# Optimization experiments

Hardware: AMD Instinct MI355X
Metric: run time of the kernel (lower is better)

Reference implementation:

```python
import jax, jax.numpy as jnp
import numpy as np

NB = 5  # frequency bands


def _ln(x, g, b, eps=1e-5):
    m = jnp.mean(x, axis=-1, keepdims=True)
    v = jnp.var(x, axis=-1, keepdims=True)
    return (x - m) / jnp.sqrt(v + eps) * g + b


def _graph_adj(x, adj_w, sw1, sb1, sw2, sb2, pos_factor, pos_enc):
    # x: [B, D, N] -> degree-normalized adjacency [B, N, N]
    d = x.shape[1]
    xt = jnp.swapaxes(x, 1, 2)  # [B, N, D]
    # concat-MLP first layer split: cat(xi, xj) @ W1 == xi @ W1[:d] + xj @ W1[d:]
    a = xt @ sw1[:d]
    bpart = xt @ sw1[d:]
    h = jax.nn.elu(a[:, :, None, :] + bpart[:, None, :, :] + sb1)  # [B, N, N, H]
    dyn = jax.nn.sigmoid(jnp.squeeze(h @ sw2, -1) + sb2)  # [B, N, N]
    static = jax.nn.softmax(adj_w, axis=-1)
    pos = jax.nn.softmax(pos_enc, axis=-1)
    comb = jax.nn.softmax(static + dyn + pos_factor * pos, axis=-1)
    deg = jnp.sum(comb, axis=-1)
    dis = (deg + 1e-8) ** -0.5
    return dis[:, :, None] * comb * dis[:, None, :]


def _gcn(x, adj, w, b):
    # x: [B, D, N], adj: [B, N, N] -> [B, D_out, N]
    xt = jnp.swapaxes(x, 1, 2)
    out = jnp.einsum('bij,bjd->bid', adj, xt) @ w + b
    return jnp.swapaxes(out, 1, 2)


def _mha(x, qkv_w, qkv_b, ow, ob, nh=4):
    B, S, D = x.shape
    dh = D // nh
    q, k, v = jnp.split(x @ qkv_w + qkv_b, 3, axis=-1)
    q = q.reshape(B, S, nh, dh)
    k = k.reshape(B, S, nh, dh)
    v = v.reshape(B, S, nh, dh)
    att = jax.nn.softmax(jnp.einsum('bihd,bjhd->bhij', q, k) / float(np.sqrt(dh)), axis=-1)
    o = jnp.einsum('bhij,bjhd->bihd', att, v).reshape(B, S, D)
    return o @ ow + ob


def setup_inputs():
    key = jax.random.key(0)
    B, D, N = 16, 256, 64
    ks = iter(jax.random.split(key, 40))

    def rn(shape, s=0.05):
        return jax.random.normal(next(ks), shape, dtype=jnp.float32) * s

    eyeN = jnp.eye(N, dtype=jnp.float32)
    return dict(
        feature=jax.random.normal(next(ks), (B, NB * D, 1, N), dtype=jnp.float32),
        l_adj_w=jnp.tile(eyeN[None], (NB, 1, 1)),
        l_sim_w1=rn((NB, 2 * D, D)), l_sim_b1=jnp.zeros((NB, D), jnp.float32),
        l_sim_w2=rn((NB, D, 1)), l_sim_b2=jnp.zeros((NB, 1), jnp.float32),
        l_pos_factor=jnp.full((NB,), 0.5, jnp.float32),
        l_pos_enc=jnp.tile(eyeN[None], (NB, 1, 1)),
        l_gcn_w=rn((NB, D, D)), l_gcn_b=jnp.zeros((NB, D), jnp.float32),
        g_adj_w=jnp.eye(NB, dtype=jnp.float32),
        g_sim_w1=rn((2 * D, D)), g_sim_b1=jnp.zeros((D,), jnp.float32),
        g_sim_w2=rn((D, 1)), g_sim_b2=jnp.zeros((1,), jnp.float32),
        g_pos_factor=jnp.float32(0.5),
        g_pos_enc=jnp.eye(NB, dtype=jnp.float32),
        g_gcn_w=rn((D, D)), g_gcn_b=jnp.zeros((D,), jnp.float32),
        qkv_w=rn((D, 3 * D)), qkv_b=jnp.zeros((3 * D,), jnp.float32),
        attn_ow=rn((D, D)), attn_ob=jnp.zeros((D,), jnp.float32),
        ln1_g=jnp.ones((D,), jnp.float32), ln1_b=jnp.zeros((D,), jnp.float32),
        ln2_g=jnp.ones((D,), jnp.float32), ln2_b=jnp.zeros((D,), jnp.float32),
        mlp_w1=rn((D, 4 * D)), mlp_b1=jnp.zeros((4 * D,), jnp.float32),
        mlp_w2=rn((4 * D, D)), mlp_b2=jnp.zeros((D,), jnp.float32),
        imp_w=rn((NB, N, 1)), imp_b=jnp.zeros((NB, 1), jnp.float32),
    )


def reference(feature, l_adj_w, l_sim_w1, l_sim_b1, l_sim_w2, l_sim_b2,
              l_pos_factor, l_pos_enc, l_gcn_w, l_gcn_b,
              g_adj_w, g_sim_w1, g_sim_b1, g_sim_w2, g_sim_b2,
              g_pos_factor, g_pos_enc, g_gcn_w, g_gcn_b,
              qkv_w, qkv_b, attn_ow, attn_ob,
              ln1_g, ln1_b, ln2_g, ln2_b,
              mlp_w1, mlp_b1, mlp_w2, mlp_b2,
              imp_w, imp_b):
    B = feature.shape[0]
    D = l_gcn_w.shape[-1]
    N = feature.shape[-1]
    # [B, 5*D, 1, N] -> [5, B, D, N] band-major
    x5 = jnp.moveaxis(feature.reshape(B, NB, D, N), 1, 0)
    # per-band local graphs + GCNs (vmapped over the 5 bands)
    local_adj = jax.vmap(_graph_adj)(x5, l_adj_w, l_sim_w1, l_sim_b1,
                                     l_sim_w2, l_sim_b2, l_pos_factor, l_pos_enc)
    local_out = jax.vmap(_gcn)(x5, local_adj, l_gcn_w, l_gcn_b)  # [5, B, D, N]
    scale_nodes = jnp.moveaxis(jnp.mean(local_out, axis=-1), 0, 1)  # [B, 5, D]
    # cross-band attention block (pre: MHA + residual + LN, then MLP + residual + LN)
    attn = _mha(scale_nodes, qkv_w, qkv_b, attn_ow, attn_ob)
    h1 = _ln(scale_nodes + attn, ln1_g, ln1_b)
    mlp = jax.nn.gelu(h1 @ mlp_w1 + mlp_b1, approximate=False) @ mlp_w2 + mlp_b2
    se = _ln(h1 + mlp, ln2_g, ln2_b)  # [B, 5, D]
    # global scale graph over the 5 band nodes
    xg = jnp.swapaxes(se, 1, 2)  # [B, D, 5]
    g_adj = _graph_adj(xg, g_adj_w, g_sim_w1, g_sim_b1, g_sim_w2, g_sim_b2,
                       g_pos_factor, g_pos_enc)
    g_out = jnp.swapaxes(_gcn(xg, g_adj, g_gcn_w, g_gcn_b), 1, 2)  # [B, 5, D]
    # modulate each local band feature by its global scale vector
    enh = local_out * jnp.moveaxis(g_out, 1, 0)[..., None]  # [5, B, D, N]
    # per-band importance projection over channels: [5, B, D, 1]
    out5 = jnp.einsum('kbdn,kno->kbdo', enh, imp_w) + imp_b[:, None, None, :]
    output = jnp.moveaxis(out5, 0, 1).reshape(B, NB * D, 1, 1)
    return output, g_adj, jnp.moveaxis(local_out, 0, 1)
```

## Files before the change

### kernel.cpp

```cpp
#include <hip/hip_runtime.h>
#include <hip/hip_bf16.h>

#define NBANDS 5
#define BATCH  16
#define DIM    256
#define NNODE  64
#define SEQ    5
#define NHEAD  4
#define DHEAD  64

typedef __hip_bfloat16 bf16;
typedef unsigned short ushort_t;
typedef __attribute__((ext_vector_type(8))) short short8;
typedef __attribute__((ext_vector_type(4))) float float4v;

__device__ __forceinline__ float bu2f(ushort_t u){
    bf16 h = *reinterpret_cast<bf16*>(&u);
    return __bfloat162float(h);
}
__device__ __forceinline__ ushort_t f2bu(float x){
    bf16 h = __float2bfloat16(x);
    return *reinterpret_cast<ushort_t*>(&h);
}

__global__ void __launch_bounds__(256) k_head(
    const float* __restrict__ l_adj_w, const float* __restrict__ l_pos_enc,
    const float* __restrict__ l_pf,
    const float* __restrict__ g_adj_w, const float* __restrict__ g_pos_enc,
    const float* __restrict__ g_pf,
    float* __restrict__ sbase, float* __restrict__ gbase,
    const float* __restrict__ w1, const float* __restrict__ gw,
    ushort_t* __restrict__ w1bt, ushort_t* __restrict__ gwbt,
    const float* __restrict__ feat,
    ushort_t* __restrict__ xtb, ushort_t* __restrict__ xtT)
{
    int blk = blockIdx.x;
    int tid = threadIdx.x;
    __shared__ ushort_t tile[64][65];

    if (blk < 80) {
        int r = blk*4 + (tid>>6);
        int k = r >> 6, i = r & 63;
        int t = tid & 63;
        float aw = l_adj_w[(k*NNODE + i)*NNODE + t];
        float pe = l_pos_enc[(k*NNODE + i)*NNODE + t];
        float m1 = aw, m2 = pe;
        for (int o=32;o>0;o>>=1){ m1 = fmaxf(m1, __shfl_xor(m1,o,64)); m2 = fmaxf(m2, __shfl_xor(m2,o,64)); }
        float e1 = __expf(aw-m1), e2 = __expf(pe-m2);
        float s1=e1, s2=e2;
        for (int o=32;o>0;o>>=1){ s1 += __shfl_xor(s1,o,64); s2 += __shfl_xor(s2,o,64); }
        float pf = l_pf[k];
        sbase[(k*NNODE+i)*NNODE + t] = e1/s1 + pf*(e2/s2);
    } else if (blk == 80) {
        if (tid < NBANDS) {
            int i = tid;
            float r1[NBANDS], r2[NBANDS];
            float m1=-1e30f, m2=-1e30f;
            for (int j=0;j<NBANDS;j++){
                r1[j]=g_adj_w[i*NBANDS+j]; r2[j]=g_pos_enc[i*NBANDS+j];
                m1=fmaxf(m1,r1[j]); m2=fmaxf(m2,r2[j]);
            }
            float s1=0.f,s2=0.f;
            for (int j=0;j<NBANDS;j++){ r1[j]=__expf(r1[j]-m1); r2[j]=__expf(r2[j]-m2); s1+=r1[j]; s2+=r2[j]; }
            float pf = g_pf[0];
            for (int j=0;j<NBANDS;j++) gbase[i*NBANDS+j] = r1[j]/s1 + pf*(r2[j]/s2);
        }
    } else if (blk < 321) {
        int idx = blk - 81;
        int inst = idx >> 4;
        int t = idx & 15;
        int r0 = (t>>2)*64, c0 = (t&3)*64;
        const float* src; ushort_t* dst;
        if (inst < 10){
            int k = inst>>1, half = inst&1;
            src = w1  + ((size_t)k*512 + half*256)*256;
            dst = w1bt+ ((size_t)k*512 + half*256)*256;
        } else {
            int k = inst-10;
            src = gw  + (size_t)k*65536;
            dst = gwbt+ (size_t)k*65536;
        }
        int jj = tid & 63, i4 = tid >> 6;
        for (int p=0;p<16;p++){
            int i = p*4 + i4;
            tile[i][jj] = f2bu(src[(size_t)(r0+i)*256 + c0 + jj]);
        }
        __syncthreads();
        for (int p=0;p<16;p++){
            int i = p*4 + i4;
            dst[(size_t)(c0+i)*256 + r0 + jj] = tile[jj][i];
        }
    } else {
        int idx = blk - 321;
        int k = idx / BATCH, b = idx % BATCH;
        const float* src = feat + ((size_t)b*NBANDS*DIM + (size_t)k*DIM)*NNODE;
        ushort_t* dst = xtb + (size_t)(k*BATCH+b)*NNODE*DIM;
        ushort_t* dstT = xtT + (size_t)(k*BATCH+b)*DIM*NNODE;
        for (int u=0; u<64; ++u){
            int i = u*256 + tid;
            dstT[i] = f2bu(src[i]);
        }
        for (int dt=0; dt<4; ++dt){
            for (int r=0;r<16;r++){
                int dp = r*4 + (tid>>6);
                int n  = tid & 63;
                tile[dp][n] = f2bu(src[(size_t)(dt*64+dp)*NNODE + n]);
            }
            __syncthreads();
            for (int r=0;r<16;r++){
                int n  = r*4 + (tid>>6);
                int dp = tid & 63;
                dst[(size_t)n*DIM + dt*64 + dp] = tile[dp][n];
            }
            __syncthreads();
        }
    }
}

__global__ void __launch_bounds__(256) k_ab_mfma(const ushort_t* __restrict__ xtb,
                        const ushort_t* __restrict__ w1bt, const float* __restrict__ b1,
                        ushort_t* __restrict__ aab, ushort_t* __restrict__ bbb)
{
    int blk = blockIdx.x;
    int kband = blk / (BATCH*8);
    int b = (blk/8) % BATCH;
    int nblk = blk & 7;
    int tid = threadIdx.x;
    int wave = tid>>6, lane = tid&63;
    int c16 = lane & 15, quad = lane >> 4;
    int m0 = wave*16;
    size_t rowbase = (size_t)(kband*BATCH+b)*NNODE;
    const ushort_t* Aptr = xtb + (rowbase + m0 + c16)*DIM + quad*8;
    const ushort_t* Bbase = w1bt + (size_t)kband*512*DIM;
    int ncol0 = nblk*64;
    const ushort_t* Bptr0 = Bbase + (size_t)(ncol0 +  0 + c16)*DIM + quad*8;
    const ushort_t* Bptr1 = Bbase + (size_t)(ncol0 + 16 + c16)*DIM + quad*8;
    const ushort_t* Bptr2 = Bbase + (size_t)(ncol0 + 32 + c16)*DIM + quad*8;
    const ushort_t* Bptr3 = Bbase + (size_t)(ncol0 + 48 + c16)*DIM + quad*8;
    float4v acc0 = {0.f,0.f,0.f,0.f}, acc1 = acc0, acc2 = acc0, acc3 = acc0;
    #pragma unroll
    for (int ks=0; ks<8; ++ks){
        short8 a  = *reinterpret_cast<const short8*>(Aptr  + ks*32);
        short8 b0 = *reinterpret_cast<const short8*>(Bptr0 + ks*32);
        short8 b1v= *reinterpret_cast<const short8*>(Bptr1 + ks*32);
        short8 b2 = *reinterpret_cast<const short8*>(Bptr2 + ks*32);
        short8 b3 = *reinterpret_cast<const short8*>(Bptr3 + ks*32);
        acc0 = __builtin_amdgcn_mfma_f32_16x16x32_bf16(a, b0, acc0, 0,0,0);
        acc1 = __builtin_amdgcn_mfma_f32_16x16x32_bf16(a, b1v, acc1, 0,0,0);
        acc2 = __builtin_amdgcn_mfma_f32_16x16x32_bf16(a, b2, acc2, 0,0,0);
        acc3 = __builtin_amdgcn_mfma_f32_16x16x32_bf16(a, b3, acc3, 0,0,0);
    }
    int half = nblk >> 2;
    int cbase = (nblk & 3)*64;
    ushort_t* dst = half ? bbb : aab;
    float4v accs[4] = {acc0, acc1, acc2, acc3};
    #pragma unroll
    for (int nt=0; nt<4; ++nt){
        int cg = cbase + nt*16 + c16;
        float bias = half ? 0.f : b1[kband*DIM + cg];
        #pragma unroll
        for (int r=0;r<4;r++){
            int m = m0 + quad*4 + r;
            dst[(rowbase + m)*DIM + cg] = f2bu(accs[nt][r] + bias);
        }
    }
}

__global__ void __launch_bounds__(256) k_dyn_comb(const ushort_t* __restrict__ aab,
                           const ushort_t* __restrict__ bbb,
                           const float* __restrict__ w2, const float* __restrict__ b2arr,
                           const float* __restrict__ sbase,
                           ushort_t* __restrict__ combb)
{
    int blk = blockIdx.x;
    int k = blk / (BATCH*16);
    int b = (blk / 16) % BATCH;
    int i0 = (blk % 16) * 4;
    int kb = k*BATCH + b;
    __shared__ ushort_t bs[64][260];
    __shared__ float arows[4][DIM];
    __shared__ float w2s[DIM];
    int tid = threadIdx.x;
    int wave = tid >> 6, lane = tid & 63;
    const ushort_t* bsrc = bbb + (size_t)kb*NNODE*DIM;
    for (int u=0; u<16; ++u){
        int idx = u*1024 + tid*4;
        int row = idx >> 8, col = idx & 255;
        *reinterpret_cast<ushort4*>(&bs[row][col]) =
            *reinterpret_cast<const ushort4*>(&bsrc[(size_t)row*DIM + col]);
    }
    for (int r=0;r<4;r++) arows[r][tid] = bu2f(aab[((size_t)kb*NNODE + i0 + r)*DIM + tid]);
    w2s[tid] = w2[k*DIM + tid];
    __syncthreads();

    int i = i0 + wave;
    float acc = 0.f;
    #pragma unroll 4
    for (int dd=0; dd<64; ++dd){
        ushort4 bv = *reinterpret_cast<const ushort4*>(&bs[lane][dd*4]);
        float4 av = *reinterpret_cast<const float4*>(&arows[wave][dd*4]);
        float4 wv = *reinterpret_cast<const float4*>(&w2s[dd*4]);
        float v0 = av.x + bu2f(bv.x);
        float v1 = av.y + bu2f(bv.y);
        float v2 = av.z + bu2f(bv.z);
        float v3 = av.w + bu2f(bv.w);
        float e0 = (v0>0.f)? v0 : (__expf(v0)-1.f);
        float e1 = (v1>0.f)? v1 : (__expf(v1)-1.f);
        float e2 = (v2>0.f)? v2 : (__expf(v2)-1.f);
        float e3 = (v3>0.f)? v3 : (__expf(v3)-1.f);
        acc += e0*wv.x + e1*wv.y + e2*wv.z + e3*wv.w;
    }
    float sb2 = b2arr[k];
    float sg = 1.f/(1.f + __expf(-(acc + sb2)));
    float val = sbase[(k*NNODE + i)*NNODE + lane] + sg;
    float m = val;
    for (int o=32;o>0;o>>=1) m = fmaxf(m, __shfl_xor(m,o,64));
    float e = __expf(val - m);
    float s = e;
    for (int o=32;o>0;o>>=1) s += __shfl_xor(s,o,64);
    combb[((size_t)kb*NNODE + i)*NNODE + lane] = f2bu(e/s);
}

__global__ void __launch_bounds__(256) k_y_mfma(const ushort_t* __restrict__ combb,
                       const ushort_t* __restrict__ xtT,
                       ushort_t* __restrict__ yb)
{
    int blk = blockIdx.x;
    int kband = blk / (BATCH*4);
    int b = (blk/4) % BATCH;
    int nblk = blk & 3;
    int tid = threadIdx.x;
    int wave = tid>>6, lane = tid&63;
    int c16 = lane & 15, quad = lane >> 4;
    int m0 = wave*16;
    int kb = kband*BATCH + b;
    const ushort_t* Aptr = combb + ((size_t)kb*NNODE + m0 + c16)*NNODE + quad*8;
    const ushort_t* Bbase = xtT + (size_t)kb*DIM*NNODE;
    int ncol0 = nblk*64;
    const ushort_t* Bptr0 = Bbase + (size_t)(ncol0 +  0 + c16)*NNODE + quad*8;
    const ushort_t* Bptr1 = Bbase + (size_t)(ncol0 + 16 + c16)*NNODE + quad*8;
    const ushort_t* Bptr2 = Bbase + (size_t)(ncol0 + 32 + c16)*NNODE + quad*8;
    const ushort_t* Bptr3 = Bbase + (size_t)(ncol0 + 48 + c16)*NNODE + quad*8;
    float4v acc0 = {0.f,0.f,0.f,0.f}, acc1 = acc0, acc2 = acc0, acc3 = acc0;
    #pragma unroll
    for (int ks=0; ks<2; ++ks){
        short8 a  = *reinterpret_cast<const short8*>(Aptr  + ks*32);
        short8 b0 = *reinterpret_cast<const short8*>(Bptr0 + ks*32);
        short8 b1v= *reinterpret_cast<const short8*>(Bptr1 + ks*32);
        short8 b2 = *reinterpret_cast<const short8*>(Bptr2 + ks*32);
        short8 b3 = *reinterpret_cast<const short8*>(Bptr3 + ks*32);
        acc0 = __builtin_amdgcn_mfma_f32_16x16x32_bf16(a, b0, acc0, 0,0,0);
        acc1 = __builtin_amdgcn_mfma_f32_16x16x32_bf16(a, b1v, acc1, 0,0,0);
        acc2 = __builtin_amdgcn_mfma_f32_16x16x32_bf16(a, b2, acc2, 0,0,0);
        acc3 = __builtin_amdgcn_mfma_f32_16x16x32_bf16(a, b3, acc3, 0,0,0);
    }
    size_t rowbase = (size_t)kb*NNODE;
    float4v accs[4] = {acc0, acc1, acc2, acc3};
    #pragma unroll
    for (int nt=0; nt<4; ++nt){
        int cg = ncol0 + nt*16 + c16;
        #pragma unroll
        for (int r=0;r<4;r++){
            int m = m0 + quad*4 + r;
            yb[(rowbase + m)*DIM + cg] = f2bu(accs[nt][r]);
        }
    }
}

__global__ void __launch_bounds__(256) k_gcn_mfma(const ushort_t* __restrict__ yb,
                         const ushort_t* __restrict__ gwbt, const float* __restrict__ gb,
                         float* __restrict__ out_local)
{
    int blk = blockIdx.x;
    int kband = blk / (BATCH*4);
    int b = (blk/4) % BATCH;
    int nblk = blk & 3;
    int tid = threadIdx.x;
    int wave = tid>>6, lane = tid&63;
    int c16 = lane & 15, quad = lane >> 4;
    int m0 = wave*16;
    int kb = kband*BATCH + b;
    const ushort_t* Aptr = yb + ((size_t)kb*NNODE + m0 + c16)*DIM + quad*8;
    const ushort_t* Bbase = gwbt + (size_t)kband*DIM*DIM;
    int ncol0 = nblk*64;
    const ushort_t* Bptr0 = Bbase + (size_t)(ncol0 +  0 + c16)*DIM + quad*8;
    const ushort_t* Bptr1 = Bbase + (size_t)(ncol0 + 16 + c16)*DIM + quad*8;
    const ushort_t* Bptr2 = Bbase + (size_t)(ncol0 + 32 + c16)*DIM + quad*8;
    const ushort_t* Bptr3 = Bbase + (size_t)(ncol0 + 48 + c16)*DIM + quad*8;
    float4v acc0 = {0.f,0.f,0.f,0.f}, acc1 = acc0, acc2 = acc0, acc3 = acc0;
    #pragma unroll
    for (int ks=0; ks<8; ++ks){
        short8 a  = *reinterpret_cast<const short8*>(Aptr  + ks*32);
        short8 b0 = *reinterpret_cast<const short8*>(Bptr0 + ks*32);
        short8 b1v= *reinterpret_cast<const short8*>(Bptr1 + ks*32);
        short8 b2 = *reinterpret_cast<const short8*>(Bptr2 + ks*32);
        short8 b3 = *reinterpret_cast<const short8*>(Bptr3 + ks*32);
        acc0 = __builtin_amdgcn_mfma_f32_16x16x32_bf16(a, b0, acc0, 0,0,0);
        acc1 = __builtin_amdgcn_mfma_f32_16x16x32_bf16(a, b1v, acc1, 0,0,0);
        acc2 = __builtin_amdgcn_mfma_f32_16x16x32_bf16(a, b2, acc2, 0,0,0);
        acc3 = __builtin_amdgcn_mfma_f32_16x16x32_bf16(a, b3, acc3, 0,0,0);
    }
    float4v accs[4] = {acc0, acc1, acc2, acc3};
    #pragma unroll
    for (int nt=0; nt<4; ++nt){
        int cg = ncol0 + nt*16 + c16;
        float bias = gb[kband*DIM + cg];
        float4 v = make_float4(accs[nt][0]+bias, accs[nt][1]+bias, accs[nt][2]+bias, accs[nt][3]+bias);
        float* dst = out_local + ((size_t)(b*NBANDS + kband)*DIM + cg)*NNODE + m0 + quad*4;
        *reinterpret_cast<float4*>(dst) = v;
    }
}

__global__ void k_scale2(const float* __restrict__ out_local, const float* __restrict__ imp_w,
                         float* __restrict__ scalew, float* __restrict__ impw)
{
    int k = blockIdx.x / BATCH, b = blockIdx.x % BATCH;
    int d = threadIdx.x;
    __shared__ float iw[NNODE];
    if (d < NNODE) iw[d] = imp_w[k*NNODE + d];
    __syncthreads();
    const float4* zl = reinterpret_cast<const float4*>(out_local + ((size_t)(b*NBANDS + k)*DIM + d)*NNODE);
    float s = 0.f, di = 0.f;
    #pragma unroll
    for (int q=0;q<16;++q){
        float4 v = zl[q];
        s  += v.x + v.y + v.z + v.w;
        di += v.x*iw[q*4] + v.y*iw[q*4+1] + v.z*iw[q*4+2] + v.w*iw[q*4+3];
    }
    scalew[((size_t)b*SEQ + k)*DIM + d] = s * (1.f/64.f);
    impw[((size_t)b*SEQ + k)*DIM + d]   = di;
}

template<int COLS, int SLICES>
__global__ void __launch_bounds__(256) k_gemv(const float* __restrict__ x, const float* __restrict__ w,
                       const float* __restrict__ bias, float* __restrict__ out,
                       int K, int N, int act)
{
    int chunks = N / COLS;
    int row = blockIdx.x / chunks;
    int n0 = (blockIdx.x % chunks) * COLS;
    int c = threadIdx.x % COLS, s = threadIdx.x / COLS;
    __shared__ float xs[1024];
    __shared__ float part[SLICES][COLS];
    for (int i = threadIdx.x; i < K; i += 256) xs[i] = x[(size_t)row*K + i];
    __syncthreads();
    int klen = K / SLICES;
    const float* wp = w + (size_t)(s*klen)*N + n0 + c;
    const float* xp = xs + s*klen;
    float acc = 0.f;
    #pragma unroll 8
    for (int i = 0; i < klen; ++i) acc += xp[i] * wp[(size_t)i*N];
    part[s][c] = acc;
    __syncthreads();
    if (s == 0){
        float v = bias[n0+c];
        #pragma unroll
        for (int q=0;q<SLICES;q++) v += part[q][c];
        if (act) v = 0.5f*v*(1.f + erff(v*0.70710678118654752f));
        out[(size_t)row*N + n0 + c] = v;
    }
}

__global__ void k_attn(const float* __restrict__ qkvw, float* __restrict__ ows)
{
    int b = blockIdx.x;
    int tid = threadIdx.x;
    int h = tid >> 6, l = tid & 63;
    __shared__ float att[NHEAD][SEQ][SEQ];
    const float* base = qkvw + (size_t)b*SEQ*3*DIM;
    for (int i=0;i<SEQ;i++){
        float qv = base[(size_t)i*3*DIM + h*DHEAD + l];
        for (int j=0;j<SEQ;j++){
            float kv = base[(size_t)j*3*DIM + DIM + h*DHEAD + l];
            float p = qv * kv;
            for (int o=32;o>0;o>>=1) p += __shfl_xor(p,o,64);
            if (l==0) att[h][i][j] = p * 0.125f;
        }
    }
    __syncthreads();
    if (l == 0){
        for (int i=0;i<SEQ;i++){
            float m=-1e30f;
            for (int j=0;j<SEQ;j++) m = fmaxf(m, att[h][i][j]);
            float e[SEQ]; float s=0.f;
            for (int j=0;j<SEQ;j++){ e[j] = __expf(att[h][i][j]-m); s+=e[j]; }
            for (int j=0;j<SEQ;j++) att[h][i][j] = e[j]/s;
        }
    }
    __syncthreads();
    for (int i=0;i<SEQ;i++){
        float acc=0.f;
        for (int j=0;j<SEQ;j++) acc += att[h][i][j] * base[(size_t)j*3*DIM + 2*DIM + h*DHEAD + l];
        ows[((size_t)b*SEQ + i)*DIM + h*DHEAD + l] = acc;
    }
}

__device__ __forceinline__ float block_ln(float v, int tid, float* red, float g, float bln)
{
    float s = v;
    for (int o=32;o>0;o>>=1) s += __shfl_xor(s,o,64);
    int wave = tid>>6, lane = tid&63;
    if (lane==0) red[wave] = s;
    __syncthreads();
    float mean = (red[0]+red[1]+red[2]+red[3]) * (1.f/DIM);
    float c = v - mean;
    float q = c*c;
    for (int o=32;o>0;o>>=1) q += __shfl_xor(q,o,64);
    __syncthreads();
    if (lane==0) red[wave] = q;
    __syncthreads();
    float var = (red[0]+red[1]+red[2]+red[3]) * (1.f/DIM);
    return c * rsqrtf(var + 1e-5f) * g + bln;
}

__global__ void __launch_bounds__(256) k_mlp1_ln(const float* __restrict__ projw,
                         const float* __restrict__ scalew,
                         const float* __restrict__ ln1_g, const float* __restrict__ ln1_b,
                         const float* __restrict__ w1, const float* __restrict__ b1,
                         float* __restrict__ h1w, float* __restrict__ mhw)
{
    int row = blockIdx.x / 16;
    int n0 = (blockIdx.x % 16) * 64;
    int tid = threadIdx.x;
    __shared__ float xs[DIM];
    __shared__ float red[4];
    __shared__ float part[4][64];
    float v = projw[(size_t)row*DIM + tid] + scalew[(size_t)row*DIM + tid];
    float h = block_ln(v, tid, red, ln1_g[tid], ln1_b[tid]);
    xs[tid] = h;
    if ((blockIdx.x % 16) == 0) h1w[(size_t)row*DIM + tid] = h;
    __syncthreads();
    int c = tid & 63, s = tid >> 6;
    const float* wp = w1 + (size_t)(s*64)*1024 + n0 + c;
    const float* xp = xs + s*64;
    float acc = 0.f;
    #pragma unroll 8
    for (int i=0;i<64;++i) acc += xp[i] * wp[(size_t)i*1024];
    part[s][c] = acc;
    __syncthreads();
    if (s == 0){
        float o = b1[n0+c] + part[0][c] + part[1][c] + part[2][c] + part[3][c];
        o = 0.5f*o*(1.f + erff(o*0.70710678118654752f));
        mhw[(size_t)row*1024 + n0 + c] = o;
    }
}

__global__ void __launch_bounds__(256) k_gab_ln(const float* __restrict__ m2w,
                        const float* __restrict__ h1w,
                        const float* __restrict__ ln2_g, const float* __restrict__ ln2_b,
                        const float* __restrict__ gw1, const float* __restrict__ gb1,
                        float* __restrict__ sew, float* __restrict__ gaw, float* __restrict__ gbw)
{
    int row = blockIdx.x / 4;
    int n0 = (blockIdx.x % 4) * 64;
    int tid = threadIdx.x;
    __shared__ float xs[DIM];
    __shared__ float red[4];
    __shared__ float partA[4][64];
    __shared__ float partB[4][64];
    float v = m2w[(size_t)row*DIM + tid] + h1w[(size_t)row*DIM + tid];
    float h = block_ln(v, tid, red, ln2_g[tid], ln2_b[tid]);
    xs[tid] = h;
    if ((blockIdx.x % 4) == 0) sew[(size_t)row*DIM + tid] = h;
    __syncthreads();
    int c = tid & 63, s = tid >> 6;
    const float* wpA = gw1 + (size_t)(s*64)*DIM + n0 + c;
    const float* wpB = wpA + (size_t)DIM*DIM;
    const float* xp = xs + s*64;
    float aA = 0.f, aB = 0.f;
    #pragma unroll 8
    for (int i=0;i<64;++i){
        float xv = xp[i];
        aA += xv * wpA[(size_t)i*DIM];
        aB += xv * wpB[(size_t)i*DIM];
    }
    partA[s][c] = aA;
    partB[s][c] = aB;
    __syncthreads();
    if (s == 0){
        gaw[(size_t)row*DIM + n0 + c] = gb1[n0+c] + partA[0][c]+partA[1][c]+partA[2][c]+partA[3][c];
        gbw[(size_t)row*DIM + n0 + c] = partB[0][c]+partB[1][c]+partB[2][c]+partB[3][c];
    }
}

__global__ void k_gadj(const float* __restrict__ gaw, const float* __restrict__ gbw,
                       const float* __restrict__ gw2, const float* __restrict__ gb2,
                       const float* __restrict__ gbase,
                       float* __restrict__ gcombw, float* __restrict__ out_gadj)
{
    int b = blockIdx.x;
    int tid = threadIdx.x;
    int wave = tid>>6, lane = tid&63;
    __shared__ float dyn[SEQ][SEQ];
    __shared__ float w2s[DIM];
    w2s[tid] = gw2[tid];
    __syncthreads();
    for (int p = wave; p < SEQ*SEQ; p += 4){
        int i = p / SEQ, j = p % SEQ;
        const float* gar = gaw + ((size_t)b*SEQ+i)*DIM;
        const float* gbr = gbw + ((size_t)b*SEQ+j)*DIM;
        float acc = 0.f;
        #pragma unroll
        for (int m=0;m<4;m++){
            int dd = lane + m*64;
            float v = gar[dd] + gbr[dd];
            float e = (v>0.f) ? v : (__expf(v)-1.f);
            acc += e * w2s[dd];
        }
        for (int o=32;o>0;o>>=1) acc += __shfl_xor(acc,o,64);
        if (lane==0) dyn[i][j] = acc;
    }
    __syncthreads();
    if (tid < SEQ){
        int i = tid;
        float sb2 = gb2[0];
        float row[SEQ]; float m=-1e30f;
        for (int j=0;j<SEQ;j++){
            float sg = 1.f/(1.f+__expf(-(dyn[i][j]+sb2)));
            row[j] = gbase[i*SEQ+j] + sg;
            m = fmaxf(m,row[j]);
        }
        float ssum=0.f;
        for (int j=0;j<SEQ;j++){ row[j]=__expf(row[j]-m); ssum+=row[j]; }
        for (int j=0;j<SEQ;j++){
            float c = row[j]/ssum;
            gcombw[((size_t)b*SEQ+i)*SEQ + j] = c;
            out_gadj[((size_t)b*SEQ+i)*SEQ + j] = c;
        }
    }
}

__global__ void __launch_bounds__(256) k_gout_mix(const float* __restrict__ gcombw,
                         const float* __restrict__ sew,
                         const float* __restrict__ ggw, const float* __restrict__ ggb,
                         float* __restrict__ goutw)
{
    int row = blockIdx.x / 4;
    int n0 = (blockIdx.x % 4) * 64;
    int b = row / SEQ;
    int tid = threadIdx.x;
    __shared__ float xs[DIM];
    __shared__ float part[4][64];
    float t = 0.f;
    #pragma unroll
    for (int j=0;j<SEQ;j++) t += gcombw[row*SEQ + j] * sew[((size_t)b*SEQ + j)*DIM + tid];
    xs[tid] = t;
    __syncthreads();
    int c = tid & 63, s = tid >> 6;
    const float* wp = ggw + (size_t)(s*64)*DIM + n0 + c;
    const float* xp = xs + s*64;
    float acc = 0.f;
    #pragma unroll 8
    for (int i=0;i<64;++i) acc += xp[i] * wp[(size_t)i*DIM];
    part[s][c] = acc;
    __syncthreads();
    if (s == 0){
        goutw[(size_t)row*DIM + n0 + c] = ggb[n0+c] + part[0][c]+part[1][c]+part[2][c]+part[3][c];
    }
}

__global__ void k_final(const float* __restrict__ impw, const float* __restrict__ goutw,
                        const float* __restrict__ imp_b, float* __restrict__ out0)
{
    int row = blockIdx.x;
    int k = row % NBANDS;
    int d = threadIdx.x;
    out0[(size_t)row*DIM + d] = goutw[(size_t)row*DIM + d] * impw[(size_t)row*DIM + d] + imp_b[k];
}

extern "C" void kernel_launch(void* const* d_in, const int* in_sizes, int n_in,
                              void* d_out, int out_size, void* d_ws, size_t ws_size,
                              hipStream_t stream)
{
    const float* feature      = (const float*)d_in[0];
    const float* l_adj_w      = (const float*)d_in[1];
    const float* l_sim_w1     = (const float*)d_in[2];
    const float* l_sim_b1     = (const float*)d_in[3];
    const float* l_sim_w2     = (const float*)d_in[4];
    const float* l_sim_b2     = (const float*)d_in[5];
    const float* l_pos_factor = (const float*)d_in[6];
    const float* l_pos_enc    = (const float*)d_in[7];
    const float* l_gcn_w      = (const float*)d_in[8];
    const float* l_gcn_b      = (const float*)d_in[9];
    const float* g_adj_w      = (const float*)d_in[10];
    const float* g_sim_w1     = (const float*)d_in[11];
    const float* g_sim_b1     = (const float*)d_in[12];
    const float* g_sim_w2     = (const float*)d_in[13];
    const float* g_sim_b2     = (const float*)d_in[14];
    const float* g_pos_factor = (const float*)d_in[15];
    const float* g_pos_enc    = (const float*)d_in[16];
    const float* g_gcn_w      = (const float*)d_in[17];
    const float* g_gcn_b      = (const float*)d_in[18];
    const float* qkv_w        = (const float*)d_in[19];
    const float* qkv_b        = (const float*)d_in[20];
    const float* attn_ow      = (const float*)d_in[21];
    const float* attn_ob      = (const float*)d_in[22];
    const float* ln1_g        = (const float*)d_in[23];
    const float* ln1_b        = (const float*)d_in[24];
    const float* ln2_g        = (const float*)d_in[25];
    const float* ln2_b        = (const float*)d_in[26];
    const float* mlp_w1       = (const float*)d_in[27];
    const float* mlp_b1       = (const float*)d_in[28];
    const float* mlp_w2       = (const float*)d_in[29];
    const float* mlp_b2       = (const float*)d_in[30];
    const float* imp_w        = (const float*)d_in[31];
    const float* imp_b        = (const float*)d_in[32];

    float* out0      = (float*)d_out;
    float* out_gadj  = out0 + (size_t)BATCH*NBANDS*DIM;
    float* out_local = out_gadj + (size_t)BATCH*NBANDS*NBANDS;

    const size_t BIG = (size_t)NBANDS*BATCH*NNODE*DIM;
    ushort_t* xtb   = (ushort_t*)d_ws;
    ushort_t* aab   = xtb + BIG;
    ushort_t* bbb   = aab + BIG;
    ushort_t* xtT   = bbb + BIG;
    ushort_t* yb    = aab;
    ushort_t* w1bt  = xtT + BIG;
    ushort_t* gwbt  = w1bt + (size_t)NBANDS*512*DIM;
    ushort_t* combb = gwbt + (size_t)NBANDS*DIM*DIM;
    float* fp = (float*)(combb + (size_t)NBANDS*BATCH*NNODE*NNODE);
    float* sbase  = fp; fp += NBANDS*NNODE*NNODE;
    float* gbase  = fp; fp += 32;
    float* scalew = fp; fp += BATCH*SEQ*DIM;
    float* impw   = fp; fp += BATCH*SEQ*DIM;
    float* qkvw   = fp; fp += BATCH*SEQ*3*DIM;
    float* ows    = fp; fp += BATCH*SEQ*DIM;
    float* projw  = fp; fp += BATCH*SEQ*DIM;
    float* h1w    = fp; fp += BATCH*SEQ*DIM;
    float* mhw    = fp; fp += BATCH*SEQ*4*DIM;
    float* m2w    = fp; fp += BATCH*SEQ*DIM;
    float* sew    = fp; fp += BATCH*SEQ*DIM;
    float* gaw    = fp; fp += BATCH*SEQ*DIM;
    float* gbw    = fp; fp += BATCH*SEQ*DIM;
    float* gcombw = fp; fp += 512;
    float* goutw  = fp; fp += BATCH*SEQ*DIM;

    const int ROWS = BATCH*SEQ;

    k_head<<<401, 256, 0, stream>>>(l_adj_w, l_pos_enc, l_pos_factor,
                                    g_adj_w, g_pos_enc, g_pos_factor,
                                    sbase, gbase,
                                    l_sim_w1, l_gcn_w, w1bt, gwbt,
                                    feature, xtb, xtT);
    k_ab_mfma<<<NBANDS*BATCH*8, 256, 0, stream>>>(xtb, w1bt, l_sim_b1, aab, bbb);
    k_dyn_comb<<<NBANDS*BATCH*16, 256, 0, stream>>>(aab, bbb, l_sim_w2, l_sim_b2, sbase, combb);
    k_y_mfma<<<NBANDS*BATCH*4, 256, 0, stream>>>(combb, xtT, yb);
    k_gcn_mfma<<<NBANDS*BATCH*4, 256, 0, stream>>>(yb, gwbt, l_gcn_b, out_local);
    k_scale2<<<NBANDS*BATCH, 256, 0, stream>>>(out_local, imp_w, scalew, impw);
    k_gemv<64,4><<<ROWS*12, 256, 0, stream>>>(scalew, qkv_w, qkv_b, qkvw, 256, 768, 0);
    k_attn<<<BATCH, 256, 0, stream>>>(qkvw, ows);
    k_gemv<64,4><<<ROWS*4, 256, 0, stream>>>(ows, attn_ow, attn_ob, projw, 256, 256, 0);
    k_mlp1_ln<<<ROWS*16, 256, 0, stream>>>(projw, scalew, ln1_g, ln1_b, mlp_w1, mlp_b1, h1w, mhw);
    k_gemv<32,8><<<ROWS*8, 256, 0, stream>>>(mhw, mlp_w2, mlp_b2, m2w, 1024, 256, 0);
    k_gab_ln<<<ROWS*4, 256, 0, stream>>>(m2w, h1w, ln2_g, ln2_b, g_sim_w1, g_sim_b1, sew, gaw, gbw);
    k_gadj<<<BATCH, 256, 0, stream>>>(gaw, gbw, g_sim_w2, g_sim_b2, gbase, gcombw, out_gadj);
    k_gout_mix<<<ROWS*4, 256, 0, stream>>>(gcombw, sew, g_gcn_w, g_gcn_b, goutw);
    k_final<<<ROWS, 256, 0, stream>>>(impw, goutw, imp_b, out0);
}
```

Measured before the change: 240.3 us.

## Fuse tail kernels and split feature conversion across more blocks

Folds the band mean and importance reduction into the GCN MFMA epilogue, which removes the separate k_scale2 pass that re-read out_local. Attention is fused with its output projection, and the global adjacency, global GCN and final modulation are merged into a single kernel, cutting the launch count from 14 to 10. Each fused block recomputes the small attention and adjacency work redundantly. The feature conversion in k_head is split over four times as many blocks (641 instead of 401) for more parallelism.

After: 218.3 us (median of 2 runs). -9.2%, faster.

```diff
diff --git a/kernel.cpp b/kernel.cpp
--- a/kernel.cpp
+++ b/kernel.cpp
@@ -92,27 +92,26 @@
         }
     } else {
         int idx = blk - 321;
-        int k = idx / BATCH, b = idx % BATCH;
+        int k = idx >> 6;
+        int b = (idx >> 2) & 15;
+        int dt = idx & 3;
         const float* src = feat + ((size_t)b*NBANDS*DIM + (size_t)k*DIM)*NNODE;
         ushort_t* dst = xtb + (size_t)(k*BATCH+b)*NNODE*DIM;
         ushort_t* dstT = xtT + (size_t)(k*BATCH+b)*DIM*NNODE;
-        for (int u=0; u<64; ++u){
-            int i = u*256 + tid;
+        for (int u=0; u<16; ++u){
+            int i = dt*4096 + u*256 + tid;
             dstT[i] = f2bu(src[i]);
         }
-        for (int dt=0; dt<4; ++dt){
-            for (int r=0;r<16;r++){
-                int dp = r*4 + (tid>>6);
-                int n  = tid & 63;
-                tile[dp][n] = f2bu(src[(size_t)(dt*64+dp)*NNODE + n]);
-            }
-            __syncthreads();
-            for (int r=0;r<16;r++){
-                int n  = r*4 + (tid>>6);
-                int dp = tid & 63;
-                dst[(size_t)n*DIM + dt*64 + dp] = tile[dp][n];
-            }
-            __syncthreads();
+        for (int r=0;r<16;r++){
+            int dp = r*4 + (tid>>6);
+            int n  = tid & 63;
+            tile[dp][n] = f2bu(src[(size_t)(dt*64+dp)*NNODE + n]);
+        }
+        __syncthreads();
+        for (int r=0;r<16;r++){
+            int n  = r*4 + (tid>>6);
+            int dp = tid & 63;
+            dst[(size_t)n*DIM + dt*64 + dp] = tile[dp][n];
         }
     }
 }
@@ -269,7 +268,9 @@
 
 __global__ void __launch_bounds__(256) k_gcn_mfma(const ushort_t* __restrict__ yb,
                          const ushort_t* __restrict__ gwbt, const float* __restrict__ gb,
-                         float* __restrict__ out_local)
+                         const float* __restrict__ imp_w,
+                         float* __restrict__ out_local,
+                         float* __restrict__ scalew, float* __restrict__ impw)
 {
     int blk = blockIdx.x;
     int kband = blk / (BATCH*4);
@@ -280,6 +281,10 @@
     int c16 = lane & 15, quad = lane >> 4;
     int m0 = wave*16;
     int kb = kband*BATCH + b;
+    __shared__ float iw_s[NNODE];
+    __shared__ float sred[4][64];
+    __shared__ float ired[4][64];
+    if (tid < NNODE) iw_s[tid] = imp_w[kband*NNODE + tid];
     const ushort_t* Aptr = yb + ((size_t)kb*NNODE + m0 + c16)*DIM + quad*8;
     const ushort_t* Bbase = gwbt + (size_t)kband*DIM*DIM;
     int ncol0 = nblk*64;
@@ -300,35 +305,34 @@
         acc2 = __builtin_amdgcn_mfma_f32_16x16x32_bf16(a, b2, acc2, 0,0,0);
         acc3 = __builtin_amdgcn_mfma_f32_16x16x32_bf16(a, b3, acc3, 0,0,0);
     }
+    __syncthreads();
     float4v accs[4] = {acc0, acc1, acc2, acc3};
     #pragma unroll
     for (int nt=0; nt<4; ++nt){
         int cg = ncol0 + nt*16 + c16;
         float bias = gb[kband*DIM + cg];
-        float4 v = make_float4(accs[nt][0]+bias, accs[nt][1]+bias, accs[nt][2]+bias, accs[nt][3]+bias);
+        float v0 = accs[nt][0]+bias, v1 = accs[nt][1]+bias, v2 = accs[nt][2]+bias, v3 = accs[nt][3]+bias;
+        float4 v = make_float4(v0, v1, v2, v3);
         float* dst = out_local + ((size_t)(b*NBANDS + kband)*DIM + cg)*NNODE + m0 + quad*4;
         *reinterpret_cast<float4*>(dst) = v;
-    }
-}
-
-__global__ void k_scale2(const float* __restrict__ out_local, const float* __restrict__ imp_w,
-                         float* __restrict__ scalew, float* __restrict__ impw)
-{
-    int k = blockIdx.x / BATCH, b = blockIdx.x % BATCH;
-    int d = threadIdx.x;
-    __shared__ float iw[NNODE];
-    if (d < NNODE) iw[d] = imp_w[k*NNODE + d];
-    __syncthreads();
-    const float4* zl = reinterpret_cast<const float4*>(out_local + ((size_t)(b*NBANDS + k)*DIM + d)*NNODE);
-    float s = 0.f, di = 0.f;
-    #pragma unroll
-    for (int q=0;q<16;++q){
-        float4 v = zl[q];
-        s  += v.x + v.y + v.z + v.w;
-        di += v.x*iw[q*4] + v.y*iw[q*4+1] + v.z*iw[q*4+2] + v.w*iw[q*4+3];
-    }
-    scalew[((size_t)b*SEQ + k)*DIM + d] = s * (1.f/64.f);
-    impw[((size_t)b*SEQ + k)*DIM + d]   = di;
+        int nb = m0 + quad*4;
+        float s  = v0 + v1 + v2 + v3;
+        float di = v0*iw_s[nb] + v1*iw_s[nb+1] + v2*iw_s[nb+2] + v3*iw_s[nb+3];
+        s  += __shfl_xor(s, 16, 64);  s  += __shfl_xor(s, 32, 64);
+        di += __shfl_xor(di, 16, 64); di += __shfl_xor(di, 32, 64);
+        if (quad == 0){
+            sred[wave][nt*16 + c16] = s;
+            ired[wave][nt*16 + c16] = di;
+        }
+    }
+    __syncthreads();
+    if (tid < 64){
+        float s  = sred[0][tid] + sred[1][tid] + sred[2][tid] + sred[3][tid];
+        float di = ired[0][tid] + ired[1][tid] + ired[2][tid] + ired[3][tid];
+        size_t o = ((size_t)b*SEQ + kband)*DIM + ncol0 + tid;
+        scalew[o] = s * (1.f/64.f);
+        impw[o]   = di;
+    }
 }
 
 template<int COLS, int SLICES>
@@ -361,37 +365,48 @@
     }
 }
 
-__global__ void k_attn(const float* __restrict__ qkvw, float* __restrict__ ows)
-{
-    int b = blockIdx.x;
+__global__ void __launch_bounds__(256) k_projattn(const float* __restrict__ qkvw,
+                        const float* __restrict__ ow, const float* __restrict__ ob,
+                        float* __restrict__ projw)
+{
+    int row = blockIdx.x / 4;
+    int n0 = (blockIdx.x % 4) * 64;
+    int b = row / SEQ, i = row % SEQ;
     int tid = threadIdx.x;
     int h = tid >> 6, l = tid & 63;
-    __shared__ float att[NHEAD][SEQ][SEQ];
+    __shared__ float xs[DIM];
+    __shared__ float part[4][64];
     const float* base = qkvw + (size_t)b*SEQ*3*DIM;
-    for (int i=0;i<SEQ;i++){
-        float qv = base[(size_t)i*3*DIM + h*DHEAD + l];
-        for (int j=0;j<SEQ;j++){
-            float kv = base[(size_t)j*3*DIM + DIM + h*DHEAD + l];
-            float p = qv * kv;
-            for (int o=32;o>0;o>>=1) p += __shfl_xor(p,o,64);
-            if (l==0) att[h][i][j] = p * 0.125f;
-        }
-    }
-    __syncthreads();
-    if (l == 0){
-        for (int i=0;i<SEQ;i++){
-            float m=-1e30f;
-            for (int j=0;j<SEQ;j++) m = fmaxf(m, att[h][i][j]);
-            float e[SEQ]; float s=0.f;
-            for (int j=0;j<SEQ;j++){ e[j] = __expf(att[h][i][j]-m); s+=e[j]; }
-            for (int j=0;j<SEQ;j++) att[h][i][j] = e[j]/s;
-        }
-    }
-    __syncthreads();
-    for (int i=0;i<SEQ;i++){
-        float acc=0.f;
-        for (int j=0;j<SEQ;j++) acc += att[h][i][j] * base[(size_t)j*3*DIM + 2*DIM + h*DHEAD + l];
-        ows[((size_t)b*SEQ + i)*DIM + h*DHEAD + l] = acc;
+    float qv = base[(size_t)i*3*DIM + h*DHEAD + l];
+    float pj[SEQ];
+    #pragma unroll
+    for (int j=0;j<SEQ;j++){
+        float p = qv * base[(size_t)j*3*DIM + DIM + h*DHEAD + l];
+        for (int o=32;o>0;o>>=1) p += __shfl_xor(p,o,64);
+        pj[j] = p * 0.125f;
+    }
+    float m = pj[0];
+    #pragma unroll
+    for (int j=1;j<SEQ;j++) m = fmaxf(m, pj[j]);
+    float ssum = 0.f;
+    #pragma unroll
+    for (int j=0;j<SEQ;j++){ pj[j] = __expf(pj[j]-m); ssum += pj[j]; }
+    float inv = 1.f/ssum;
+    float o = 0.f;
+    #pragma unroll
+    for (int j=0;j<SEQ;j++) o += pj[j]*inv * base[(size_t)j*3*DIM + 2*DIM + h*DHEAD + l];
+    xs[tid] = o;
+    __syncthreads();
+    int c = tid & 63, s = tid >> 6;
+    const float* wp = ow + (size_t)(s*64)*DIM + n0 + c;
+    const float* xp = xs + s*64;
+    float acc = 0.f;
+    #pragma unroll 8
+    for (int k=0;k<64;++k) acc += xp[k] * wp[(size_t)k*DIM];
+    part[s][c] = acc;
+    __syncthreads();
+    if (s == 0){
+        projw[(size_t)row*DIM + n0 + c] = ob[n0+c] + part[0][c]+part[1][c]+part[2][c]+part[3][c];
     }
 }
 
@@ -483,67 +498,59 @@
     }
 }
 
-__global__ void k_gadj(const float* __restrict__ gaw, const float* __restrict__ gbw,
-                       const float* __restrict__ gw2, const float* __restrict__ gb2,
-                       const float* __restrict__ gbase,
-                       float* __restrict__ gcombw, float* __restrict__ out_gadj)
-{
-    int b = blockIdx.x;
-    int tid = threadIdx.x;
-    int wave = tid>>6, lane = tid&63;
-    __shared__ float dyn[SEQ][SEQ];
-    __shared__ float w2s[DIM];
-    w2s[tid] = gw2[tid];
-    __syncthreads();
-    for (int p = wave; p < SEQ*SEQ; p += 4){
-        int i = p / SEQ, j = p % SEQ;
-        const float* gar = gaw + ((size_t)b*SEQ+i)*DIM;
-        const float* gbr = gbw + ((size_t)b*SEQ+j)*DIM;
+__global__ void __launch_bounds__(256) k_goutfin(const float* __restrict__ gaw,
+                        const float* __restrict__ gbw,
+                        const float* __restrict__ gw2, const float* __restrict__ gb2,
+                        const float* __restrict__ gbase,
+                        const float* __restrict__ sew,
+                        const float* __restrict__ ggw, const float* __restrict__ ggb,
+                        const float* __restrict__ impw, const float* __restrict__ imp_b,
+                        float* __restrict__ out0, float* __restrict__ out_gadj)
+{
+    int row = blockIdx.x / 4;
+    int n0 = (blockIdx.x % 4) * 64;
+    int b = row / SEQ, i = row % SEQ;
+    int tid = threadIdx.x;
+    int wave = tid >> 6, lane = tid & 63;
+    __shared__ float dyn_s[SEQ];
+    __shared__ float xs[DIM];
+    __shared__ float part[4][64];
+    for (int j = wave; j < SEQ; j += 4){
+        const float* gar = gaw + (size_t)row*DIM;
+        const float* gbr = gbw + ((size_t)b*SEQ + j)*DIM;
         float acc = 0.f;
         #pragma unroll
         for (int m=0;m<4;m++){
             int dd = lane + m*64;
             float v = gar[dd] + gbr[dd];
             float e = (v>0.f) ? v : (__expf(v)-1.f);
-            acc += e * w2s[dd];
+            acc += e * gw2[dd];
         }
         for (int o=32;o>0;o>>=1) acc += __shfl_xor(acc,o,64);
-        if (lane==0) dyn[i][j] = acc;
-    }
-    __syncthreads();
-    if (tid < SEQ){
-        int i = tid;
+        if (lane==0) dyn_s[j] = acc;
+    }
+    __syncthreads();
+    float gc[SEQ];
+    {
         float sb2 = gb2[0];
-        float row[SEQ]; float m=-1e30f;
+        float m = -1e30f;
+        #pragma unroll
         for (int j=0;j<SEQ;j++){
-            float sg = 1.f/(1.f+__expf(-(dyn[i][j]+sb2)));
-            row[j] = gbase[i*SEQ+j] + sg;
-            m = fmaxf(m,row[j]);
+            float sg = 1.f/(1.f+__expf(-(dyn_s[j]+sb2)));
+            gc[j] = gbase[i*SEQ+j] + sg;
+            m = fmaxf(m, gc[j]);
         }
         float ssum=0.f;
-        for (int j=0;j<SEQ;j++){ row[j]=__expf(row[j]-m); ssum+=row[j]; }
-        for (int j=0;j<SEQ;j++){
-            float c = row[j]/ssum;
-            gcombw[((size_t)b*SEQ+i)*SEQ + j] = c;
-            out_gadj[((size_t)b*SEQ+i)*SEQ + j] = c;
-        }
-    }
-}
-
-__global__ void __launch_bounds__(256) k_gout_mix(const float* __restrict__ gcombw,
-                         const float* __restrict__ sew,
-                         const float* __restrict__ ggw, const float* __restrict__ ggb,
-                         float* __restrict__ goutw)
-{
-    int row = blockIdx.x / 4;
-    int n0 = (blockIdx.x % 4) * 64;
-    int b = row / SEQ;
-    int tid = threadIdx.x;
-    __shared__ float xs[DIM];
-    __shared__ float part[4][64];
+        #pragma unroll
+        for (int j=0;j<SEQ;j++){ gc[j]=__expf(gc[j]-m); ssum+=gc[j]; }
+        float inv = 1.f/ssum;
+        #pragma unroll
+        for (int j=0;j<SEQ;j++) gc[j] *= inv;
+    }
+    if (n0 == 0 && tid < SEQ) out_gadj[((size_t)b*SEQ+i)*SEQ + tid] = gc[tid];
     float t = 0.f;
     #pragma unroll
-    for (int j=0;j<SEQ;j++) t += gcombw[row*SEQ + j] * sew[((size_t)b*SEQ + j)*DIM + tid];
+    for (int j=0;j<SEQ;j++) t += gc[j]*sew[((size_t)b*SEQ + j)*DIM + tid];
     xs[tid] = t;
     __syncthreads();
     int c = tid & 63, s = tid >> 6;
@@ -551,21 +558,14 @@
     const float* xp = xs + s*64;
     float acc = 0.f;
     #pragma unroll 8
-    for (int i=0;i<64;++i) acc += xp[i] * wp[(size_t)i*DIM];
+    for (int k=0;k<64;++k) acc += xp[k] * wp[(size_t)k*DIM];
     part[s][c] = acc;
     __syncthreads();
     if (s == 0){
-        goutw[(size_t)row*DIM + n0 + c] = ggb[n0+c] + part[0][c]+part[1][c]+part[2][c]+part[3][c];
-    }
-}
-
-__global__ void k_final(const float* __restrict__ impw, const float* __restrict__ goutw,
-                        const float* __restrict__ imp_b, float* __restrict__ out0)
-{
-    int row = blockIdx.x;
-    int k = row % NBANDS;
-    int d = threadIdx.x;
-    out0[(size_t)row*DIM + d] = goutw[(size_t)row*DIM + d] * impw[(size_t)row*DIM + d] + imp_b[k];
+        float g = ggb[n0+c] + part[0][c]+part[1][c]+part[2][c]+part[3][c];
+        size_t o = (size_t)row*DIM + n0 + c;
+        out0[o] = g * impw[o] + imp_b[i];
+    }
 }
 
 extern "C" void kernel_launch(void* const* d_in, const int* in_sizes, int n_in,
@@ -625,7 +625,6 @@
     float* scalew = fp; fp += BATCH*SEQ*DIM;
     float* impw   = fp; fp += BATCH*SEQ*DIM;
     float* qkvw   = fp; fp += BATCH*SEQ*3*DIM;
-    float* ows    = fp; fp += BATCH*SEQ*DIM;
     float* projw  = fp; fp += BATCH*SEQ*DIM;
     float* h1w    = fp; fp += BATCH*SEQ*DIM;
     float* mhw    = fp; fp += BATCH*SEQ*4*DIM;
@@ -633,12 +632,10 @@
     float* sew    = fp; fp += BATCH*SEQ*DIM;
     float* gaw    = fp; fp += BATCH*SEQ*DIM;
     float* gbw    = fp; fp += BATCH*SEQ*DIM;
-    float* gcombw = fp; fp += 512;
-    float* goutw  = fp; fp += BATCH*SEQ*DIM;
 
     const int ROWS = BATCH*SEQ;
 
-    k_head<<<401, 256, 0, stream>>>(l_adj_w, l_pos_enc, l_pos_factor,
+    k_head<<<641, 256, 0, stream>>>(l_adj_w, l_pos_enc, l_pos_factor,
                                     g_adj_w, g_pos_enc, g_pos_factor,
                                     sbase, gbase,
                                     l_sim_w1, l_gcn_w, w1bt, gwbt,
@@ -646,15 +643,14 @@
     k_ab_mfma<<<NBANDS*BATCH*8, 256, 0, stream>>>(xtb, w1bt, l_sim_b1, aab, bbb);
     k_dyn_comb<<<NBANDS*BATCH*16, 256, 0, stream>>>(aab, bbb, l_sim_w2, l_sim_b2, sbase, combb);
     k_y_mfma<<<NBANDS*BATCH*4, 256, 0, stream>>>(combb, xtT, yb);
-    k_gcn_mfma<<<NBANDS*BATCH*4, 256, 0, stream>>>(yb, gwbt, l_gcn_b, out_local);
-    k_scale2<<<NBANDS*BATCH, 256, 0, stream>>>(out_local, imp_w, scalew, impw);
+    k_gcn_mfma<<<NBANDS*BATCH*4, 256, 0, stream>>>(yb, gwbt, l_gcn_b, imp_w,
+                                                   out_local, scalew, impw);
     k_gemv<64,4><<<ROWS*12, 256, 0, stream>>>(scalew, qkv_w, qkv_b, qkvw, 256, 768, 0);
-    k_attn<<<BATCH, 256, 0, stream>>>(qkvw, ows);
-    k_gemv<64,4><<<ROWS*4, 256, 0, stream>>>(ows, attn_ow, attn_ob, projw, 256, 256, 0);
+    k_projattn<<<ROWS*4, 256, 0, stream>>>(qkvw, attn_ow, attn_ob, projw);
     k_mlp1_ln<<<ROWS*16, 256, 0, stream>>>(projw, scalew, ln1_g, ln1_b, mlp_w1, mlp_b1, h1w, mhw);
     k_gemv<32,8><<<ROWS*8, 256, 0, stream>>>(mhw, mlp_w2, mlp_b2, m2w, 1024, 256, 0);
     k_gab_ln<<<ROWS*4, 256, 0, stream>>>(m2w, h1w, ln2_g, ln2_b, g_sim_w1, g_sim_b1, sew, gaw, gbw);
-    k_gadj<<<BATCH, 256, 0, stream>>>(gaw, gbw, g_sim_w2, g_sim_b2, gbase, gcombw, out_gadj);
-    k_gout_mix<<<ROWS*4, 256, 0, stream>>>(gcombw, sew, g_gcn_w, g_gcn_b, goutw);
-    k_final<<<ROWS, 256, 0, stream>>>(impw, goutw, imp_b, out0);
-}
+    k_goutfin<<<ROWS*4, 256, 0, stream>>>(gaw, gbw, g_sim_w2, g_sim_b2, gbase,
+                                          sew, g_gcn_w, g_gcn_b, impw, imp_b,
+                                          out0, out_gadj);
+}
```
